# Optimization experiments

Hardware: AMD Instinct MI355X
Metric: run time of the kernel (lower is better)

## Reference

```python
import jax, jax.numpy as jnp
import numpy as np


def setup_inputs() -> dict:
    key = jax.random.key(0)
    kx, ky = jax.random.split(key)
    B, N, M, D = 4, 8192, 8192, 3
    x = jax.random.normal(kx, (B, N, D), dtype=jnp.float32)
    y = jax.random.normal(ky, (B, M, D), dtype=jnp.float32)
    return {"x": x, "y": y}


def reference(x, y):
    # Pairwise squared distances: [B, N, M]
    x2 = jnp.sum(x * x, axis=-1)  # [B, N]
    y2 = jnp.sum(y * y, axis=-1)  # [B, M]
    xy = jnp.einsum("bnd,bmd->bnm", x, y)  # [B, N, M]
    d2 = x2[:, :, None] + y2[:, None, :] - 2.0 * xy
    # Chamfer: min over the other set in each direction
    min_xy = jnp.min(d2, axis=2)  # [B, N] nearest y for each x
    min_yx = jnp.min(d2, axis=1)  # [B, M] nearest x for each y
    return jnp.mean(min_xy) + jnp.mean(min_yx)
```

## Files before the change

### kernel.cpp

```cpp
#include <hip/hip_runtime.h>

#define BATCHES 4
#define NPTS    8192
#define INF32   3.0e38f

typedef _Float16 f16x8  __attribute__((ext_vector_type(8)));
typedef float    f32x16 __attribute__((ext_vector_type(16)));

__device__ inline void fsplit(float v, _Float16& h, _Float16& l) {
    h = (_Float16)v;
    l = (_Float16)(v - (float)h);
}

__global__ __launch_bounds__(256) void chamfer_prep(
    const float* __restrict__ x, const float* __restrict__ y,
    _Float16* __restrict__ pA, _Float16* __restrict__ pB,
    int* __restrict__ mininit )
{
    int i = blockIdx.x * 256 + threadIdx.x;
    mininit[i]         = 0x7F7F7F7F;
    mininit[i + 32768] = 0x7F7F7F7F;

    const float* xp = x + (size_t)i * 3;
    const float* yp = y + (size_t)i * 3;
    float x0 = xp[0], x1 = xp[1], x2 = xp[2];
    float y0 = yp[0], y1 = yp[1], y2 = yp[2];

    _Float16 xh[3], xl[3], yh[3], yl[3];
    fsplit(x0, xh[0], xl[0]); fsplit(x1, xh[1], xl[1]); fsplit(x2, xh[2], xl[2]);
    fsplit(y0, yh[0], yl[0]); fsplit(y1, yh[1], yl[1]); fsplit(y2, yh[2], yl[2]);

    float q = fmaf(x2, x2, fmaf(x1, x1, x0 * x0));
    float s = fmaf(y2, y2, fmaf(y1, y1, y0 * y0));
    _Float16 qh, ql, sh, sl;
    fsplit(q, qh, ql); fsplit(s, sh, sl);

    __align__(16) _Float16 av[16];
    __align__(16) _Float16 bv[16];
    #pragma unroll
    for (int k = 0; k < 3; ++k) {
        av[k]     = xh[k];
        av[3 + k] = xl[k];
        av[6 + k] = xh[k];
        bv[k]     = (_Float16)(-2.0f * (float)yh[k]);
        bv[3 + k] = bv[k];
        bv[6 + k] = (_Float16)(-2.0f * (float)yl[k]);
    }
    av[9] = qh; av[10] = ql; av[11] = (_Float16)1.0f; av[12] = (_Float16)1.0f;
    bv[9] = (_Float16)1.0f; bv[10] = (_Float16)1.0f; bv[11] = sh; bv[12] = sl;
    av[13] = av[14] = av[15] = (_Float16)0.0f;
    bv[13] = bv[14] = bv[15] = (_Float16)0.0f;

    int4* dA = (int4*)(pA + (size_t)i * 16);
    int4* dB = (int4*)(pB + (size_t)i * 16);
    dA[0] = ((int4*)av)[0]; dA[1] = ((int4*)av)[1];
    dB[0] = ((int4*)bv)[0]; dB[1] = ((int4*)bv)[1];
}

__global__ __launch_bounds__(256, 4) void chamfer_mfma(
    const _Float16* __restrict__ pA, const _Float16* __restrict__ pB,
    float* __restrict__ rowfinal,
    float* __restrict__ colfinal)
{
    int bid   = blockIdx.x;
    int b     = bid >> 9;
    int rem   = bid & 511;
    int strip = rem >> 3;
    int cr    = rem & 7;
    int tid   = threadIdx.x;
    int wv    = tid >> 6, lane = tid & 63;
    int lo    = lane & 31, hi = lane >> 5;

    const _Float16* Ab = pA + (size_t)b * NPTS * 16;
    const _Float16* Bb = pB + (size_t)b * NPTS * 16;
    int rw = strip * 128 + wv * 32;
    int c0 = cr * 1024;

    __shared__ int colmin[1024];
    for (int i = tid; i < 1024; i += 256) colmin[i] = 0x7F7F7F7F;
    __syncthreads();

    f16x8 af = *(const f16x8*)(Ab + (size_t)(rw + lo) * 16 + hi * 8);

    float rmin[16];
    #pragma unroll
    for (int r = 0; r < 16; ++r) rmin[r] = INF32;

    const f32x16 zero = {0.f,0.f,0.f,0.f,0.f,0.f,0.f,0.f,
                         0.f,0.f,0.f,0.f,0.f,0.f,0.f,0.f};

    auto loadB = [&](int t) -> f16x8 {
        return *(const f16x8*)(Bb + (size_t)(c0 + ((t & 31) << 5) + lo) * 16 + hi * 8);
    };

#define COLCHAIN(C, V)                                   \
    float C = fminf(fminf(V[0], V[1]), V[2]);            \
    C = fminf(fminf(C, V[3]),  V[4]);                    \
    C = fminf(fminf(C, V[5]),  V[6]);                    \
    C = fminf(fminf(C, V[7]),  V[8]);                    \
    C = fminf(fminf(C, V[9]),  V[10]);                   \
    C = fminf(fminf(C, V[11]), V[12]);                   \
    C = fminf(fminf(C, V[13]), V[14]);                   \
    C = fminf(C, V[15]);

#define CHAMFER_BODY(P, Q, TT)                                                  \
    {                                                                           \
        f32x16 A = __builtin_amdgcn_mfma_f32_32x32x16_f16(af, P, zero, 0, 0, 0);\
        f32x16 B = __builtin_amdgcn_mfma_f32_32x32x16_f16(af, Q, zero, 0, 0, 0);\
        _Pragma("unroll")                                                       \
        for (int r = 0; r < 16; ++r)                                            \
            rmin[r] = fminf(fminf(A[r], B[r]), rmin[r]);            \
        COLCHAIN(ca, A)                                                         \
        COLCHAIN(cb, B)                                                         \
        ca = fminf(ca, __shfl_xor(ca, 32, 64));                                 \
        cb = fminf(cb, __shfl_xor(cb, 32, 64));                                 \
               \
        float cw  = (hi == 0) ? ca : cb;                                        \
        int   cix = (((TT) + hi) << 5) + lo;                                    \
        atomicMin(&colmin[cix], __float_as_int(fmaxf(cw, 0.f)));                \
    }

    f16x8 p0 = loadB(0), p1 = loadB(1);
    #pragma unroll 1
    for (int t = 0; t < 32; t += 4) {
        f16x8 q0 = loadB(t + 2), q1 = loadB(t + 3);
        CHAMFER_BODY(p0, p1, t)
        p0 = loadB(t + 4); p1 = loadB(t + 5);
        CHAMFER_BODY(q0, q1, t + 2)
    }
#undef CHAMFER_BODY
#undef COLCHAIN

    #pragma unroll
    for (int r = 0; r < 16; ++r) {
        float v = rmin[r];
        v = fminf(v, __shfl_xor(v, 1, 64));
        v = fminf(v, __shfl_xor(v, 2, 64));
        v = fminf(v, __shfl_xor(v, 4, 64));
        v = fminf(v, __shfl_xor(v, 8, 64));
        v = fminf(v, __shfl_xor(v, 16, 64));
        if (lo == 0) {
            int row = rw + (r & 3) + ((r >> 2) << 3) + (hi << 2);
            atomicMin((int*)&rowfinal[b * NPTS + row],
                      __float_as_int(fmaxf(v, 0.f)));
        }
    }

    __syncthreads();
    for (int i = tid; i < 1024; i += 256)
        atomicMin((int*)&colfinal[b * NPTS + c0 + i], colmin[i]);
}

__global__ __launch_bounds__(256) void chamfer_reduce1(
    const float* __restrict__ minbuf, double* __restrict__ partials)
{
    int base = blockIdx.x * 1024 + threadIdx.x * 4;
    float4 v = *reinterpret_cast<const float4*>(minbuf + base);
    double s = ((double)v.x + (double)v.y) + ((double)v.z + (double)v.w);
    #pragma unroll
    for (int off = 32; off > 0; off >>= 1) s += __shfl_down(s, off, 64);
    __shared__ double sd[4];
    int wid = threadIdx.x >> 6;
    if ((threadIdx.x & 63) == 0) sd[wid] = s;
    __syncthreads();
    if (threadIdx.x == 0)
        partials[blockIdx.x] = (sd[0] + sd[1]) + (sd[2] + sd[3]);
}

__global__ __launch_bounds__(64) void chamfer_reduce2(
    const double* __restrict__ partials, float* __restrict__ out)
{
    double s = partials[threadIdx.x];
    #pragma unroll
    for (int off = 32; off > 0; off >>= 1) s += __shfl_down(s, off, 64);
    if (threadIdx.x == 0)
        out[0] = (float)(s / (double)(BATCHES * NPTS));
}

extern "C" void kernel_launch(void* const* d_in, const int* in_sizes, int n_in,
                              void* d_out, int out_size, void* d_ws, size_t ws_size,
                              hipStream_t stream)
{
    const float* x = (const float*)d_in[0];
    const float* y = (const float*)d_in[1];
    float* out = (float*)d_out;

    float*    rowfinal = (float*)d_ws;
    float*    colfinal = rowfinal + 32768;
    _Float16* pA = (_Float16*)(colfinal + 32768);
    _Float16* pB = pA + (size_t)BATCHES * NPTS * 16;
    double*   partials = (double*)(pB + (size_t)BATCHES * NPTS * 16);

    chamfer_prep<<<BATCHES * NPTS / 256, 256, 0, stream>>>(x, y, pA, pB,
                                                           (int*)rowfinal);
    chamfer_mfma<<<2048, 256, 0, stream>>>(pA, pB, rowfinal, colfinal);
    chamfer_reduce1<<<64, 256, 0, stream>>>(rowfinal, partials);
    chamfer_reduce2<<<1, 64, 0, stream>>>(partials, out);
}
```

Baseline: 36.73 us.

## Compute both chamfer directions as separate row-min passes, dropping column reductions

Replaces the combined row/column min reduction with two independent passes (x→y and y→x), each doing only row minima over its MFMA tiles. This removes the per-tile column fmin chains, cross-lane shuffles and LDS atomicMin traffic, and each wave now processes two 32-row A fragments per B load for more reuse. The cost is doubling the MFMA work and packing both point sets in both A and B forms during prep.

```diff
diff --git a/kernel.cpp b/kernel.cpp
--- a/kernel.cpp
+++ b/kernel.cpp
@@ -12,9 +12,40 @@
     l = (_Float16)(v - (float)h);
 }
 
+__device__ inline void pack_point(float p0, float p1, float p2,
+                                  _Float16* __restrict__ avec,
+                                  _Float16* __restrict__ bvec)
+{
+    _Float16 h[3], l[3];
+    fsplit(p0, h[0], l[0]); fsplit(p1, h[1], l[1]); fsplit(p2, h[2], l[2]);
+    float q = fmaf(p2, p2, fmaf(p1, p1, p0 * p0));
+    _Float16 qh, ql;
+    fsplit(q, qh, ql);
+
+    __align__(16) _Float16 av[16];
+    __align__(16) _Float16 bv[16];
+    #pragma unroll
+    for (int k = 0; k < 3; ++k) {
+        av[k]     = h[k];
+        av[3 + k] = l[k];
+        av[6 + k] = h[k];
+        bv[k]     = (_Float16)(-2.0f * (float)h[k]);
+        bv[3 + k] = bv[k];
+        bv[6 + k] = (_Float16)(-2.0f * (float)l[k]);
+    }
+    av[9] = qh; av[10] = ql; av[11] = (_Float16)1.0f; av[12] = (_Float16)1.0f;
+    bv[9] = (_Float16)1.0f; bv[10] = (_Float16)1.0f; bv[11] = qh; bv[12] = ql;
+    av[13] = av[14] = av[15] = (_Float16)0.0f;
+    bv[13] = bv[14] = bv[15] = (_Float16)0.0f;
+
+    ((int4*)avec)[0] = ((int4*)av)[0]; ((int4*)avec)[1] = ((int4*)av)[1];
+    ((int4*)bvec)[0] = ((int4*)bv)[0]; ((int4*)bvec)[1] = ((int4*)bv)[1];
+}
+
 __global__ __launch_bounds__(256) void chamfer_prep(
     const float* __restrict__ x, const float* __restrict__ y,
-    _Float16* __restrict__ pA, _Float16* __restrict__ pB,
+    _Float16* __restrict__ pAx, _Float16* __restrict__ pBx,
+    _Float16* __restrict__ pAy, _Float16* __restrict__ pBy,
     int* __restrict__ mininit )
 {
     int i = blockIdx.x * 256 + threadIdx.x;
@@ -23,132 +54,87 @@
 
     const float* xp = x + (size_t)i * 3;
     const float* yp = y + (size_t)i * 3;
-    float x0 = xp[0], x1 = xp[1], x2 = xp[2];
-    float y0 = yp[0], y1 = yp[1], y2 = yp[2];
-
-    _Float16 xh[3], xl[3], yh[3], yl[3];
-    fsplit(x0, xh[0], xl[0]); fsplit(x1, xh[1], xl[1]); fsplit(x2, xh[2], xl[2]);
-    fsplit(y0, yh[0], yl[0]); fsplit(y1, yh[1], yl[1]); fsplit(y2, yh[2], yl[2]);
-
-    float q = fmaf(x2, x2, fmaf(x1, x1, x0 * x0));
-    float s = fmaf(y2, y2, fmaf(y1, y1, y0 * y0));
-    _Float16 qh, ql, sh, sl;
-    fsplit(q, qh, ql); fsplit(s, sh, sl);
-
-    __align__(16) _Float16 av[16];
-    __align__(16) _Float16 bv[16];
-    #pragma unroll
-    for (int k = 0; k < 3; ++k) {
-        av[k]     = xh[k];
-        av[3 + k] = xl[k];
-        av[6 + k] = xh[k];
-        bv[k]     = (_Float16)(-2.0f * (float)yh[k]);
-        bv[3 + k] = bv[k];
-        bv[6 + k] = (_Float16)(-2.0f * (float)yl[k]);
-    }
-    av[9] = qh; av[10] = ql; av[11] = (_Float16)1.0f; av[12] = (_Float16)1.0f;
-    bv[9] = (_Float16)1.0f; bv[10] = (_Float16)1.0f; bv[11] = sh; bv[12] = sl;
-    av[13] = av[14] = av[15] = (_Float16)0.0f;
-    bv[13] = bv[14] = bv[15] = (_Float16)0.0f;
-
-    int4* dA = (int4*)(pA + (size_t)i * 16);
-    int4* dB = (int4*)(pB + (size_t)i * 16);
-    dA[0] = ((int4*)av)[0]; dA[1] = ((int4*)av)[1];
-    dB[0] = ((int4*)bv)[0]; dB[1] = ((int4*)bv)[1];
+    pack_point(xp[0], xp[1], xp[2], pAx + (size_t)i * 16, pBx + (size_t)i * 16);
+    pack_point(yp[0], yp[1], yp[2], pAy + (size_t)i * 16, pBy + (size_t)i * 16);
 }
 
 __global__ __launch_bounds__(256, 4) void chamfer_mfma(
-    const _Float16* __restrict__ pA, const _Float16* __restrict__ pB,
-    float* __restrict__ rowfinal,
-    float* __restrict__ colfinal)
+    const _Float16* __restrict__ pAx, const _Float16* __restrict__ pBx,
+    const _Float16* __restrict__ pAy, const _Float16* __restrict__ pBy,
+    float* __restrict__ minall )
 {
     int bid   = blockIdx.x;
-    int b     = bid >> 9;
+    int dir   = bid >> 9;
     int rem   = bid & 511;
-    int strip = rem >> 3;
-    int cr    = rem & 7;
+    int b     = rem >> 7;
+    int rem2  = rem & 127;
+    int strip = rem2 >> 2;
+    int chunk = rem2 & 3;
     int tid   = threadIdx.x;
     int wv    = tid >> 6, lane = tid & 63;
     int lo    = lane & 31, hi = lane >> 5;
 
-    const _Float16* Ab = pA + (size_t)b * NPTS * 16;
-    const _Float16* Bb = pB + (size_t)b * NPTS * 16;
-    int rw = strip * 128 + wv * 32;
-    int c0 = cr * 1024;
+    const _Float16* Adata = ((dir == 0) ? pAx : pAy) + (size_t)b * NPTS * 16;
+    const _Float16* Bdata = ((dir == 0) ? pBy : pBx) + (size_t)b * NPTS * 16;
+    float* outMin = minall + ((size_t)dir << 15) + (size_t)b * NPTS;
 
-    __shared__ int colmin[1024];
-    for (int i = tid; i < 1024; i += 256) colmin[i] = 0x7F7F7F7F;
-    __syncthreads();
+    int rw = strip * 256 + wv * 64;
+    int c0 = chunk * 2048;
 
-    f16x8 af = *(const f16x8*)(Ab + (size_t)(rw + lo) * 16 + hi * 8);
+    f16x8 af0 = *(const f16x8*)(Adata + (size_t)(rw + lo) * 16 + hi * 8);
+    f16x8 af1 = *(const f16x8*)(Adata + (size_t)(rw + 32 + lo) * 16 + hi * 8);
 
-    float rmin[16];
+    float rmin0[16], rmin1[16];
     #pragma unroll
-    for (int r = 0; r < 16; ++r) rmin[r] = INF32;
+    for (int r = 0; r < 16; ++r) { rmin0[r] = INF32; rmin1[r] = INF32; }
 
     const f32x16 zero = {0.f,0.f,0.f,0.f,0.f,0.f,0.f,0.f,
                          0.f,0.f,0.f,0.f,0.f,0.f,0.f,0.f};
 
     auto loadB = [&](int t) -> f16x8 {
-        return *(const f16x8*)(Bb + (size_t)(c0 + ((t & 31) << 5) + lo) * 16 + hi * 8);
+        return *(const f16x8*)(Bdata + (size_t)(c0 + (t << 5) + lo) * 16 + hi * 8);
     };
 
-#define COLCHAIN(C, V)                                   \
-    float C = fminf(fminf(V[0], V[1]), V[2]);            \
-    C = fminf(fminf(C, V[3]),  V[4]);                    \
-    C = fminf(fminf(C, V[5]),  V[6]);                    \
-    C = fminf(fminf(C, V[7]),  V[8]);                    \
-    C = fminf(fminf(C, V[9]),  V[10]);                   \
-    C = fminf(fminf(C, V[11]), V[12]);                   \
-    C = fminf(fminf(C, V[13]), V[14]);                   \
-    C = fminf(C, V[15]);
-
-#define CHAMFER_BODY(P, Q, TT)                                                  \
-    {                                                                           \
-        f32x16 A = __builtin_amdgcn_mfma_f32_32x32x16_f16(af, P, zero, 0, 0, 0);\
-        f32x16 B = __builtin_amdgcn_mfma_f32_32x32x16_f16(af, Q, zero, 0, 0, 0);\
-        _Pragma("unroll")                                                       \
-        for (int r = 0; r < 16; ++r)                                            \
-            rmin[r] = fminf(fminf(A[r], B[r]), rmin[r]);            \
-        COLCHAIN(ca, A)                                                         \
-        COLCHAIN(cb, B)                                                         \
-        ca = fminf(ca, __shfl_xor(ca, 32, 64));                                 \
-        cb = fminf(cb, __shfl_xor(cb, 32, 64));                                 \
-               \
-        float cw  = (hi == 0) ? ca : cb;                                        \
-        int   cix = (((TT) + hi) << 5) + lo;                                    \
-        atomicMin(&colmin[cix], __float_as_int(fmaxf(cw, 0.f)));                \
+    f16x8 b0 = loadB(0), b1 = loadB(1);
+    #pragma unroll 1
+    for (int t = 0; t < 64; t += 2) {
+        f16x8 n0 = loadB((t + 2) & 63);
+        f16x8 n1 = loadB((t + 3) & 63);
+        f32x16 A0 = __builtin_amdgcn_mfma_f32_32x32x16_f16(af0, b0, zero, 0, 0, 0);
+        f32x16 A1 = __builtin_amdgcn_mfma_f32_32x32x16_f16(af0, b1, zero, 0, 0, 0);
+        #pragma unroll
+        for (int r = 0; r < 16; ++r)
+            rmin0[r] = fminf(fminf(A0[r], A1[r]), rmin0[r]);
+        f32x16 B0 = __builtin_amdgcn_mfma_f32_32x32x16_f16(af1, b0, zero, 0, 0, 0);
+        f32x16 B1 = __builtin_amdgcn_mfma_f32_32x32x16_f16(af1, b1, zero, 0, 0, 0);
+        #pragma unroll
+        for (int r = 0; r < 16; ++r)
+            rmin1[r] = fminf(fminf(B0[r], B1[r]), rmin1[r]);
+        b0 = n0; b1 = n1;
     }
-
-    f16x8 p0 = loadB(0), p1 = loadB(1);
-    #pragma unroll 1
-    for (int t = 0; t < 32; t += 4) {
-        f16x8 q0 = loadB(t + 2), q1 = loadB(t + 3);
-        CHAMFER_BODY(p0, p1, t)
-        p0 = loadB(t + 4); p1 = loadB(t + 5);
-        CHAMFER_BODY(q0, q1, t + 2)
-    }
-#undef CHAMFER_BODY
-#undef COLCHAIN
 
     #pragma unroll
     for (int r = 0; r < 16; ++r) {
-        float v = rmin[r];
+        float v = rmin0[r];
         v = fminf(v, __shfl_xor(v, 1, 64));
         v = fminf(v, __shfl_xor(v, 2, 64));
         v = fminf(v, __shfl_xor(v, 4, 64));
         v = fminf(v, __shfl_xor(v, 8, 64));
         v = fminf(v, __shfl_xor(v, 16, 64));
+        float w = rmin1[r];
+        w = fminf(w, __shfl_xor(w, 1, 64));
+        w = fminf(w, __shfl_xor(w, 2, 64));
+        w = fminf(w, __shfl_xor(w, 4, 64));
+        w = fminf(w, __shfl_xor(w, 8, 64));
+        w = fminf(w, __shfl_xor(w, 16, 64));
         if (lo == 0) {
-            int row = rw + (r & 3) + ((r >> 2) << 3) + (hi << 2);
-            atomicMin((int*)&rowfinal[b * NPTS + row],
+            int rr = (r & 3) + ((r >> 2) << 3) + (hi << 2);
+            atomicMin((int*)&outMin[rw + rr],
                       __float_as_int(fmaxf(v, 0.f)));
+            atomicMin((int*)&outMin[rw + 32 + rr],
+                      __float_as_int(fmaxf(w, 0.f)));
         }
     }
-
-    __syncthreads();
-    for (int i = tid; i < 1024; i += 256)
-        atomicMin((int*)&colfinal[b * NPTS + c0 + i], colmin[i]);
 }
 
 __global__ __launch_bounds__(256) void chamfer_reduce1(
@@ -185,15 +171,16 @@
     const float* y = (const float*)d_in[1];
     float* out = (float*)d_out;
 
-    float*    rowfinal = (float*)d_ws;
-    float*    colfinal = rowfinal + 32768;
-    _Float16* pA = (_Float16*)(colfinal + 32768);
-    _Float16* pB = pA + (size_t)BATCHES * NPTS * 16;
-    double*   partials = (double*)(pB + (size_t)BATCHES * NPTS * 16);
+    float*    minall = (float*)d_ws;
+    _Float16* pAx = (_Float16*)(minall + 65536);
+    _Float16* pBx = pAx + (size_t)BATCHES * NPTS * 16;
+    _Float16* pAy = pBx + (size_t)BATCHES * NPTS * 16;
+    _Float16* pBy = pAy + (size_t)BATCHES * NPTS * 16;
+    double*   partials = (double*)(pBy + (size_t)BATCHES * NPTS * 16);
 
-    chamfer_prep<<<BATCHES * NPTS / 256, 256, 0, stream>>>(x, y, pA, pB,
-                                                           (int*)rowfinal);
-    chamfer_mfma<<<2048, 256, 0, stream>>>(pA, pB, rowfinal, colfinal);
-    chamfer_reduce1<<<64, 256, 0, stream>>>(rowfinal, partials);
+    chamfer_prep<<<BATCHES * NPTS / 256, 256, 0, stream>>>(
+        x, y, pAx, pBx, pAy, pBy, (int*)minall);
+    chamfer_mfma<<<1024, 256, 0, stream>>>(pAx, pBx, pAy, pBy, minall);
+    chamfer_reduce1<<<64, 256, 0, stream>>>(minall, partials);
     chamfer_reduce2<<<1, 64, 0, stream>>>(partials, out);
 }
```

Result: slower. 39.37 us (+7.2%).
